# Optimization experiments

Measured on AMD Instinct MI355X. Metric: run time of the kernel, lower is better.

## Reference

```python
import jax, jax.numpy as jnp
import numpy as np

EPS = 1e-8  # epsilon from padded_softmax


def setup_inputs() -> dict:
    key = jax.random.key(0)
    k1, k2 = jax.random.split(key)
    B, N, NC = 32, 1024, 3
    C = jax.random.normal(k1, (B, N, NC), dtype=jnp.float32)
    masks = jnp.ones((B, N, N), dtype=jnp.float32)
    # nn.Parameter(torch.rand(1) * 0.02 + 0.99)
    inverse_sigma = jax.random.uniform(k2, (1,), dtype=jnp.float32) * 0.02 + 0.99
    return {"C": C, "masks": masks, "inverse_sigma": inverse_sigma}


def reference(C, masks, inverse_sigma):
    # Pairwise squared euclidean distances via the Gram-matrix identity
    # ||x-y||^2 = ||x||^2 + ||y||^2 - 2<x,y>  (avoids the [B,N,N,NC] expand).
    sq = jnp.sum(C * C, axis=-1)                                  # [B, N]
    gram = jnp.einsum('bnc,bmc->bnm', C, C)                       # [B, N, N]
    D = sq[:, :, None] + sq[:, None, :] - 2.0 * gram              # [B, N, N]
    # Gaussian kernel adjacency.
    A = jnp.exp(-(inverse_sigma ** 2) * D)                        # [B, N, N]
    # padded_softmax: exp(-A) * masks, normalized along last axis.
    X = jnp.exp(-A) * masks
    return X / (jnp.sum(X, axis=-1, keepdims=True) + EPS)
```

## Files before the change

### kernel.cpp

```cpp
#include <hip/hip_runtime.h>

#define EPS 1e-8f
#define LOG2E 1.4426950408889634f

typedef float f32x4 __attribute__((ext_vector_type(4)));

#define CALC(c0, c1, c2, mval, cn0, cn1, cn2, sqn, k1)           \
    ({                                                           \
        float _sqm = (c0)*(c0) + (c1)*(c1) + (c2)*(c2);          \
        float _dot = (cn0)*(c0) + (cn1)*(c1) + (cn2)*(c2);       \
        float _D   = (sqn) + _sqm - 2.0f * _dot;                 \
        float _A   = __builtin_amdgcn_exp2f((k1) * _D);          \
        __builtin_amdgcn_exp2f(-LOG2E * _A) * (mval);            \
    })

__global__ __launch_bounds__(256) void gaussian_rownorm_1024(
    const float* __restrict__ C,
    const float* __restrict__ masks,
    const float* __restrict__ inv_sigma,
    float* __restrict__ out)
{
    constexpr int N = 1024;
    const int wid  = threadIdx.x >> 6;
    const int lane = threadIdx.x & 63;
    const int row  = blockIdx.x * 4 + wid;
    const int b    = row >> 10;
    const int n    = row & (N - 1);

    const float s  = inv_sigma[0];
    const float k1 = -(s * s) * LOG2E;

    const float* __restrict__ Cb = C + (size_t)b * N * 3;
    const float cn0 = Cb[n * 3 + 0];
    const float cn1 = Cb[n * 3 + 1];
    const float cn2 = Cb[n * 3 + 2];
    const float sqn = cn0 * cn0 + cn1 * cn1 + cn2 * cn2;

    const size_t rowbase = (size_t)row * N;

    f32x4 mk[4];
    #pragma unroll
    for (int k = 0; k < 4; ++k)
        mk[k] = __builtin_nontemporal_load(
            (const f32x4*)(masks + rowbase + k * 256 + lane * 4));

    float x[16];
    float psum = 0.0f;
    #pragma unroll
    for (int k = 0; k < 4; ++k) {
        const int m0 = k * 256 + lane * 4;
        const f32x4* __restrict__ cm = (const f32x4*)(Cb + m0 * 3);
        const f32x4 ca  = cm[0];
        const f32x4 cb4 = cm[1];
        const f32x4 cc  = cm[2];

        x[k*4+0] = CALC(ca.x,  ca.y,  ca.z,  mk[k].x, cn0, cn1, cn2, sqn, k1);
        x[k*4+1] = CALC(ca.w,  cb4.x, cb4.y, mk[k].y, cn0, cn1, cn2, sqn, k1);
        x[k*4+2] = CALC(cb4.z, cb4.w, cc.x,  mk[k].z, cn0, cn1, cn2, sqn, k1);
        x[k*4+3] = CALC(cc.y,  cc.z,  cc.w,  mk[k].w, cn0, cn1, cn2, sqn, k1);
        psum += (x[k*4+0] + x[k*4+1]) + (x[k*4+2] + x[k*4+3]);
    }

    #pragma unroll
    for (int off = 32; off > 0; off >>= 1)
        psum += __shfl_xor(psum, off, 64);

    const float r = 1.0f / (psum + EPS);

    #pragma unroll
    for (int k = 0; k < 4; ++k) {
        f32x4 o;
        o.x = x[k*4+0] * r; o.y = x[k*4+1] * r;
        o.z = x[k*4+2] * r; o.w = x[k*4+3] * r;
        __builtin_nontemporal_store(o, (f32x4*)(out + rowbase + k * 256 + lane * 4));
    }
}

__global__ __launch_bounds__(256) void gaussian_rownorm_generic(
    const float* __restrict__ C,
    const float* __restrict__ masks,
    const float* __restrict__ inv_sigma,
    float* __restrict__ out,
    int N)
{
    const int n = blockIdx.x;
    const int b = blockIdx.y;
    const int t = threadIdx.x;

    const float s  = inv_sigma[0];
    const float k1 = -(s * s) * LOG2E;

    const float* __restrict__ Cb = C + (size_t)b * N * 3;
    const float cn0 = Cb[n * 3 + 0];
    const float cn1 = Cb[n * 3 + 1];
    const float cn2 = Cb[n * 3 + 2];
    const float sqn = cn0 * cn0 + cn1 * cn1 + cn2 * cn2;

    const int m0 = t * 4;
    const f32x4* __restrict__ cm = (const f32x4*)(Cb + (size_t)m0 * 3);
    const f32x4 ca  = cm[0];
    const f32x4 cb4 = cm[1];
    const f32x4 cc  = cm[2];

    const size_t rowbase = ((size_t)b * N + n) * N;
    const f32x4 mk = __builtin_nontemporal_load((const f32x4*)(masks + rowbase + m0));

    const float x0 = CALC(ca.x,  ca.y,  ca.z,  mk.x, cn0, cn1, cn2, sqn, k1);
    const float x1 = CALC(ca.w,  cb4.x, cb4.y, mk.y, cn0, cn1, cn2, sqn, k1);
    const float x2 = CALC(cb4.z, cb4.w, cc.x,  mk.z, cn0, cn1, cn2, sqn, k1);
    const float x3 = CALC(cc.y,  cc.z,  cc.w,  mk.w, cn0, cn1, cn2, sqn, k1);

    float psum = (x0 + x1) + (x2 + x3);
    #pragma unroll
    for (int off = 32; off > 0; off >>= 1)
        psum += __shfl_xor(psum, off, 64);

    __shared__ float wsum[4];
    const int wid = t >> 6;
    if ((t & 63) == 0) wsum[wid] = psum;
    __syncthreads();

    const float total = wsum[0] + wsum[1] + wsum[2] + wsum[3];
    const float r = 1.0f / (total + EPS);

    f32x4 o;
    o.x = x0 * r; o.y = x1 * r; o.z = x2 * r; o.w = x3 * r;
    __builtin_nontemporal_store(o, (f32x4*)(out + rowbase + m0));
}

extern "C" void kernel_launch(void* const* d_in, const int* in_sizes, int n_in,
                              void* d_out, int out_size, void* d_ws, size_t ws_size,
                              hipStream_t stream) {
    const float* C         = (const float*)d_in[0];
    const float* masks     = (const float*)d_in[1];
    const float* inv_sigma = (const float*)d_in[2];
    float* out             = (float*)d_out;

    const long long N_ll = (long long)out_size * 3LL / (long long)in_sizes[0];
    const int N = (int)N_ll;
    const int B = in_sizes[0] / (3 * N);

    if (N == 1024 && (B * N) % 4 == 0) {
        const int grid = B * N / 4;
        gaussian_rownorm_1024<<<grid, 256, 0, stream>>>(C, masks, inv_sigma, out);
    } else {
        dim3 grid(N, B);
        gaussian_rownorm_generic<<<grid, N / 4, 0, stream>>>(C, masks, inv_sigma, out, N);
    }
}
```

Baseline: 233.0 us.

## Process four rows per wave, reusing C columns and double-buffering mask loads

Each wave now handles four consecutive rows instead of one. It loads the column coordinates of C once into registers and reuses them across all four rows. Mask loads are software-pipelined: the next row's masks are fetched while the current row is computed, and they switch from nontemporal to regular loads. This cuts redundant C loads and launches a quarter as many blocks, at the cost of higher register pressure and fewer waves for hiding latency.

```diff
diff --git a/kernel.cpp b/kernel.cpp
--- a/kernel.cpp
+++ b/kernel.cpp
@@ -5,14 +5,44 @@
 
 typedef float f32x4 __attribute__((ext_vector_type(4)));
 
-#define CALC(c0, c1, c2, mval, cn0, cn1, cn2, sqn, k1)           \
-    ({                                                           \
-        float _sqm = (c0)*(c0) + (c1)*(c1) + (c2)*(c2);          \
-        float _dot = (cn0)*(c0) + (cn1)*(c1) + (cn2)*(c2);       \
-        float _D   = (sqn) + _sqm - 2.0f * _dot;                 \
-        float _A   = __builtin_amdgcn_exp2f((k1) * _D);          \
-        __builtin_amdgcn_exp2f(-LOG2E * _A) * (mval);            \
-    })
+__device__ __forceinline__ float calcx(float c0, float c1, float c2, float mval,
+                                       float cn0, float cn1, float cn2,
+                                       float sqn, float k1) {
+    float sqm = c0*c0 + c1*c1 + c2*c2;
+    float dot = cn0*c0 + cn1*c1 + cn2*c2;
+    float D   = sqn + sqm - 2.0f*dot;
+    float A   = __builtin_amdgcn_exp2f(k1 * D);
+    return __builtin_amdgcn_exp2f(-LOG2E * A) * mval;
+}
+
+__device__ __forceinline__ void do_row(const f32x4 (&cm)[12],
+                                       f32x4 m0, f32x4 m1, f32x4 m2, f32x4 m3,
+                                       float cn0, float cn1, float cn2,
+                                       float sqn, float k1,
+                                       float* __restrict__ outp) {
+    float x[16];
+    float ps = 0.0f;
+    #pragma unroll
+    for (int k = 0; k < 4; ++k) {
+        const f32x4 a = cm[k*3+0], b = cm[k*3+1], c = cm[k*3+2];
+        const f32x4 mv = (k == 0) ? m0 : (k == 1) ? m1 : (k == 2) ? m2 : m3;
+        x[k*4+0] = calcx(a.x, a.y, a.z, mv.x, cn0, cn1, cn2, sqn, k1);
+        x[k*4+1] = calcx(a.w, b.x, b.y, mv.y, cn0, cn1, cn2, sqn, k1);
+        x[k*4+2] = calcx(b.z, b.w, c.x, mv.z, cn0, cn1, cn2, sqn, k1);
+        x[k*4+3] = calcx(c.y, c.z, c.w, mv.w, cn0, cn1, cn2, sqn, k1);
+        ps += (x[k*4+0] + x[k*4+1]) + (x[k*4+2] + x[k*4+3]);
+    }
+    #pragma unroll
+    for (int off = 32; off > 0; off >>= 1)
+        ps += __shfl_xor(ps, off, 64);
+    const float r = 1.0f / (ps + EPS);
+    #pragma unroll
+    for (int k = 0; k < 4; ++k) {
+        f32x4 o;
+        o.x = x[k*4+0]*r; o.y = x[k*4+1]*r; o.z = x[k*4+2]*r; o.w = x[k*4+3]*r;
+        __builtin_nontemporal_store(o, (f32x4*)(outp + k*256));
+    }
+}
 
 __global__ __launch_bounds__(256) void gaussian_rownorm_1024(
     const float* __restrict__ C,
@@ -23,57 +53,52 @@
     constexpr int N = 1024;
     const int wid  = threadIdx.x >> 6;
     const int lane = threadIdx.x & 63;
-    const int row  = blockIdx.x * 4 + wid;
-    const int b    = row >> 10;
-    const int n    = row & (N - 1);
+    const int row0 = (blockIdx.x * 4 + wid) * 4;
+    const int b    = row0 >> 10;
 
     const float s  = inv_sigma[0];
     const float k1 = -(s * s) * LOG2E;
 
     const float* __restrict__ Cb = C + (size_t)b * N * 3;
-    const float cn0 = Cb[n * 3 + 0];
-    const float cn1 = Cb[n * 3 + 1];
-    const float cn2 = Cb[n * 3 + 2];
-    const float sqn = cn0 * cn0 + cn1 * cn1 + cn2 * cn2;
 
-    const size_t rowbase = (size_t)row * N;
-
-    f32x4 mk[4];
-    #pragma unroll
-    for (int k = 0; k < 4; ++k)
-        mk[k] = __builtin_nontemporal_load(
-            (const f32x4*)(masks + rowbase + k * 256 + lane * 4));
-
-    float x[16];
-    float psum = 0.0f;
+    f32x4 cm[12];
     #pragma unroll
     for (int k = 0; k < 4; ++k) {
-        const int m0 = k * 256 + lane * 4;
-        const f32x4* __restrict__ cm = (const f32x4*)(Cb + m0 * 3);
-        const f32x4 ca  = cm[0];
-        const f32x4 cb4 = cm[1];
-        const f32x4 cc  = cm[2];
-
-        x[k*4+0] = CALC(ca.x,  ca.y,  ca.z,  mk[k].x, cn0, cn1, cn2, sqn, k1);
-        x[k*4+1] = CALC(ca.w,  cb4.x, cb4.y, mk[k].y, cn0, cn1, cn2, sqn, k1);
-        x[k*4+2] = CALC(cb4.z, cb4.w, cc.x,  mk[k].z, cn0, cn1, cn2, sqn, k1);
-        x[k*4+3] = CALC(cc.y,  cc.z,  cc.w,  mk[k].w, cn0, cn1, cn2, sqn, k1);
-        psum += (x[k*4+0] + x[k*4+1]) + (x[k*4+2] + x[k*4+3]);
+        const f32x4* p = (const f32x4*)(Cb + (size_t)(k*256 + lane*4) * 3);
+        cm[k*3+0] = p[0]; cm[k*3+1] = p[1]; cm[k*3+2] = p[2];
     }
 
+    float cn0[4], cn1[4], cn2[4], sqn[4];
     #pragma unroll
-    for (int off = 32; off > 0; off >>= 1)
-        psum += __shfl_xor(psum, off, 64);
+    for (int r = 0; r < 4; ++r) {
+        const int n = (row0 + r) & (N - 1);
+        cn0[r] = Cb[n*3+0]; cn1[r] = Cb[n*3+1]; cn2[r] = Cb[n*3+2];
+        sqn[r] = cn0[r]*cn0[r] + cn1[r]*cn1[r] + cn2[r]*cn2[r];
+    }
 
-    const float r = 1.0f / (psum + EPS);
+    const float* mbase = masks + (size_t)row0 * N + lane * 4;
+    float*       obase = out   + (size_t)row0 * N + lane * 4;
 
-    #pragma unroll
-    for (int k = 0; k < 4; ++k) {
-        f32x4 o;
-        o.x = x[k*4+0] * r; o.y = x[k*4+1] * r;
-        o.z = x[k*4+2] * r; o.w = x[k*4+3] * r;
-        __builtin_nontemporal_store(o, (f32x4*)(out + rowbase + k * 256 + lane * 4));
-    }
+    #define LOADM(d0, d1, d2, d3, r) do {                         \
+        const float* _p = mbase + (size_t)(r) * N;                \
+        d0 = *(const f32x4*)(_p +   0);                           \
+        d1 = *(const f32x4*)(_p + 256);                           \
+        d2 = *(const f32x4*)(_p + 512);                           \
+        d3 = *(const f32x4*)(_p + 768);                           \
+    } while (0)
+
+    f32x4 a0, a1, a2, a3;
+    f32x4 b0, b1, b2, b3;
+
+    LOADM(a0, a1, a2, a3, 0);
+    LOADM(b0, b1, b2, b3, 1);
+    do_row(cm, a0, a1, a2, a3, cn0[0], cn1[0], cn2[0], sqn[0], k1, obase + 0*N);
+    LOADM(a0, a1, a2, a3, 2);
+    do_row(cm, b0, b1, b2, b3, cn0[1], cn1[1], cn2[1], sqn[1], k1, obase + 1*N);
+    LOADM(b0, b1, b2, b3, 3);
+    do_row(cm, a0, a1, a2, a3, cn0[2], cn1[2], cn2[2], sqn[2], k1, obase + 2*N);
+    do_row(cm, b0, b1, b2, b3, cn0[3], cn1[3], cn2[3], sqn[3], k1, obase + 3*N);
+    #undef LOADM
 }
 
 __global__ __launch_bounds__(256) void gaussian_rownorm_generic(
@@ -97,18 +122,18 @@
     const float sqn = cn0 * cn0 + cn1 * cn1 + cn2 * cn2;
 
     const int m0 = t * 4;
-    const f32x4* __restrict__ cm = (const f32x4*)(Cb + (size_t)m0 * 3);
-    const f32x4 ca  = cm[0];
-    const f32x4 cb4 = cm[1];
-    const f32x4 cc  = cm[2];
+    const f32x4* __restrict__ cmp = (const f32x4*)(Cb + (size_t)m0 * 3);
+    const f32x4 ca  = cmp[0];
+    const f32x4 cb4 = cmp[1];
+    const f32x4 cc  = cmp[2];
 
     const size_t rowbase = ((size_t)b * N + n) * N;
-    const f32x4 mk = __builtin_nontemporal_load((const f32x4*)(masks + rowbase + m0));
+    const f32x4 mk = *(const f32x4*)(masks + rowbase + m0);
 
-    const float x0 = CALC(ca.x,  ca.y,  ca.z,  mk.x, cn0, cn1, cn2, sqn, k1);
-    const float x1 = CALC(ca.w,  cb4.x, cb4.y, mk.y, cn0, cn1, cn2, sqn, k1);
-    const float x2 = CALC(cb4.z, cb4.w, cc.x,  mk.z, cn0, cn1, cn2, sqn, k1);
-    const float x3 = CALC(cc.y,  cc.z,  cc.w,  mk.w, cn0, cn1, cn2, sqn, k1);
+    const float x0 = calcx(ca.x,  ca.y,  ca.z,  mk.x, cn0, cn1, cn2, sqn, k1);
+    const float x1 = calcx(ca.w,  cb4.x, cb4.y, mk.y, cn0, cn1, cn2, sqn, k1);
+    const float x2 = calcx(cb4.z, cb4.w, cc.x,  mk.z, cn0, cn1, cn2, sqn, k1);
+    const float x3 = calcx(cc.y,  cc.z,  cc.w,  mk.w, cn0, cn1, cn2, sqn, k1);
 
     float psum = (x0 + x1) + (x2 + x3);
     #pragma unroll
@@ -140,8 +165,8 @@
     const int N = (int)N_ll;
     const int B = in_sizes[0] / (3 * N);
 
-    if (N == 1024 && (B * N) % 4 == 0) {
-        const int grid = B * N / 4;
+    if (N == 1024 && (B * N) % 16 == 0) {
+        const int grid = B * N / 16;
         gaussian_rownorm_1024<<<grid, 256, 0, stream>>>(C, masks, inv_sigma, out);
     } else {
         dim3 grid(N, B);
```

Measured after the change: 232.8 us. No clear change (-0.1%).
